# Kernel optimization log

Measured on AMD Instinct MI355X. Metric: run time of the kernel, lower is better.

The kernel has to match this reference:

```python
import jax, jax.numpy as jnp
import numpy as np

N = 2_000_000   # points
C = 65_536      # cluster centers
F = 8           # point feature dim
D = 3           # coord dim


def _dense_params(key, din, dout):
    kw, kb = jax.random.split(key)
    scale = jnp.sqrt(2.0 / din).astype(jnp.float32)
    return (jax.random.normal(kw, (din, dout), jnp.float32) * scale,
            jnp.zeros((dout,), jnp.float32))


def setup_inputs() -> dict:
    key = jax.random.key(0)
    ks = jax.random.split(key, 16)
    inp = {
        "point_features": jax.random.normal(ks[0], (N, F), jnp.float32),
        "labels": jax.random.randint(ks[1], (N,), 0, C, jnp.int32),
        "cluster_centers": jax.random.normal(ks[2], (C, D), jnp.float32),
        "points": jax.random.normal(ks[3], (N, D), jnp.float32),
    }
    # edge MLP: (F+D)->8->16->32->64
    dims = [F + D, 8, 16, 32, 64]
    for i in range(4):
        w, b = _dense_params(ks[4 + i], dims[i], dims[i + 1])
        inp[f"we{i}"] = w
        inp[f"be{i}"] = b
    # attention MLP: (F+D)->64->1
    inp["wa0"], inp["ba0"] = _dense_params(ks[8], F + D, 64)
    inp["wa1"], inp["ba1"] = _dense_params(ks[9], 64, 1)
    # output MLP: 64->128->256
    inp["wo0"], inp["bo0"] = _dense_params(ks[10], 64, 128)
    inp["wo1"], inp["bo1"] = _dense_params(ks[11], 128, 256)
    return inp


def reference(point_features, labels, cluster_centers, points,
              we0, be0, we1, be1, we2, be2, we3, be3,
              wa0, ba0, wa1, ba1, wo0, bo0, wo1, bo1):
    relu = jax.nn.relu
    # gather center coords for each point, build edge input [N, F+D]
    center_coords = cluster_centers[labels]
    x = jnp.concatenate([point_features, center_coords - points], axis=-1)
    # edge MLP 8->16->32->64 (all relu)
    h = relu(x @ we0 + be0)
    h = relu(h @ we1 + be1)
    h = relu(h @ we2 + be2)
    h = relu(h @ we3 + be3)            # [N, 64]
    # attention MLP 64->1 sigmoid
    a = relu(x @ wa0 + ba0)
    a = jax.nn.sigmoid(a @ wa1 + ba1)  # [N, 1]
    t = h * a
    # scatter-sum into clusters
    agg = jax.ops.segment_sum(t, labels, num_segments=C)  # [C, 64]
    # output MLP 128->256 (relu, relu)
    o = relu(agg @ wo0 + bo0)
    o = relu(o @ wo1 + bo1)            # [C, 256]
    return o
```

## Files before the change

### kernel.cpp

```cpp
#include <hip/hip_runtime.h>
#include <hip/hip_bf16.h>
#include <math.h>
#include <stdint.h>

#define TPB 256
#define NCB 32
#define SAGG_LD 68
#define SMID_LD 132

typedef float f32x4 __attribute__((ext_vector_type(4)));
typedef short bf16x8 __attribute__((ext_vector_type(8)));

__device__ inline unsigned int bf16bits(float f)
{
    __hip_bfloat16 b = __float2bfloat16(f);
    return (unsigned int)(*(unsigned short*)&b);
}

__global__ __launch_bounds__(TPB) void hist_kernel(
    const int* __restrict__ labels, int* __restrict__ counts, int n)
{
    int i = blockIdx.x * TPB + threadIdx.x;
    if (i < n) atomicAdd(&counts[labels[i]], 1);
}

__global__ __launch_bounds__(256) void scan_local(
    const int* __restrict__ counts, int* __restrict__ off,
    int* __restrict__ bsum, int C)
{
    __shared__ int sh[256];
    int t = threadIdx.x;
    int i = blockIdx.x * 256 + t;
    int v = (i < C) ? counts[i] : 0;
    sh[t] = v;
    __syncthreads();
    for (int d = 1; d < 256; d <<= 1) {
        int u = (t >= d) ? sh[t - d] : 0;
        __syncthreads();
        sh[t] += u;
        __syncthreads();
    }
    if (i < C) off[i] = sh[t] - v;
    if (t == 255) bsum[blockIdx.x] = sh[255];
}

__global__ __launch_bounds__(256) void scan_base(
    int* __restrict__ bsum, int* __restrict__ off, int nb, int C)
{
    __shared__ int sh[256];
    int t = threadIdx.x;
    int v = (t < nb) ? bsum[t] : 0;
    sh[t] = v;
    __syncthreads();
    for (int d = 1; d < 256; d <<= 1) {
        int u = (t >= d) ? sh[t - d] : 0;
        __syncthreads();
        sh[t] += u;
        __syncthreads();
    }
    if (t < nb) bsum[t] = sh[t] - v;
    if (t == 255) off[C] = sh[255];
}

__global__ __launch_bounds__(256) void scan_apply(
    int* __restrict__ off, int* __restrict__ cursor,
    const int* __restrict__ bsum, int C)
{
    int i = blockIdx.x * 256 + threadIdx.x;
    if (i < C) {
        int v = off[i] + bsum[blockIdx.x];
        off[i] = v;
        cursor[i] = v;
    }
}

__global__ __launch_bounds__(TPB, 4) void point_mlp_kernel(
    const float* __restrict__ pf, const int* __restrict__ labels,
    const float* __restrict__ centers, const float* __restrict__ points,
    const float* __restrict__ we0, const float* __restrict__ be0,
    const float* __restrict__ we1, const float* __restrict__ be1,
    const float* __restrict__ we2, const float* __restrict__ be2,
    const float* __restrict__ we3, const float* __restrict__ be3,
    const float* __restrict__ wa0, const float* __restrict__ ba0,
    const float* __restrict__ wa1, const float* __restrict__ ba1,
    int* __restrict__ cursor, unsigned short* __restrict__ tsort, int n)
{
    __shared__ unsigned int s_h3[4][16][64];

    int i0 = blockIdx.x * TPB + threadIdx.x;
    int i  = (i0 < n) ? i0 : (n - 1);

    float x[11];
    const float4* pf4 = (const float4*)pf;
    float4 p0 = pf4[(size_t)i * 2 + 0];
    float4 p1 = pf4[(size_t)i * 2 + 1];
    x[0] = p0.x; x[1] = p0.y; x[2] = p0.z; x[3] = p0.w;
    x[4] = p1.x; x[5] = p1.y; x[6] = p1.z; x[7] = p1.w;

    int lbl = labels[i];
    x[8]  = centers[lbl * 3 + 0] - points[(size_t)i * 3 + 0];
    x[9]  = centers[lbl * 3 + 1] - points[(size_t)i * 3 + 1];
    x[10] = centers[lbl * 3 + 2] - points[(size_t)i * 3 + 2];

    int pos = 0;
    if (i0 < n) pos = atomicAdd(&cursor[lbl], 1);

    float s = ba1[0];
#pragma unroll
    for (int j = 0; j < 64; j++) {
        float aj = ba0[j];
#pragma unroll
        for (int k = 0; k < 11; k++) aj = fmaf(x[k], wa0[k * 64 + j], aj);
        aj = fmaxf(aj, 0.f);
        s = fmaf(aj, wa1[j], s);
    }
    float gate = 1.f / (1.f + __expf(-s));

    float h1[8];
#pragma unroll
    for (int j = 0; j < 8; j++) {
        float v = be0[j];
#pragma unroll
        for (int k = 0; k < 11; k++) v = fmaf(x[k], we0[k * 8 + j], v);
        h1[j] = fmaxf(v, 0.f);
    }
    float h2[16];
#pragma unroll
    for (int j = 0; j < 16; j++) {
        float v = be1[j];
#pragma unroll
        for (int k = 0; k < 8; k++) v = fmaf(h1[k], we1[k * 16 + j], v);
        h2[j] = fmaxf(v, 0.f);
    }
    float h3[32];
#pragma unroll
    for (int j = 0; j < 32; j++) {
        float v = be2[j];
#pragma unroll
        for (int k = 0; k < 16; k++) v = fmaf(h2[k], we2[k * 32 + j], v);
        h3[j] = fmaxf(v, 0.f);
    }

    int lane = threadIdx.x & 63;
    int w    = threadIdx.x >> 6;
    int lg   = lane >> 4;
    int lm   = lane & 15;
    int pbase = blockIdx.x * TPB + w * 64;

#pragma unroll
    for (int kk = 0; kk < 16; kk++) {
        s_h3[w][kk][lane] = bf16bits(h3[2 * kk]) | (bf16bits(h3[2 * kk + 1]) << 16);
    }

    bf16x8 afrag[4];
#pragma unroll
    for (int mt = 0; mt < 4; mt++) {
        union { unsigned int u[4]; bf16x8 v; } au;
#pragma unroll
        for (int ii = 0; ii < 4; ii++) {
            float w0 = we3[(lg * 8 + 2 * ii + 0) * 64 + mt * 16 + lm];
            float w1 = we3[(lg * 8 + 2 * ii + 1) * 64 + mt * 16 + lm];
            au.u[ii] = bf16bits(w0) | (bf16bits(w1) << 16);
        }
        afrag[mt] = au.v;
    }

#pragma unroll
    for (int nt = 0; nt < 4; nt++) {
        int   spt  = nt * 16 + lm;
        float g    = __shfl(gate, spt, 64);
        int   ppos = __shfl(pos,  spt, 64);
        bool  valid = (pbase + spt) < n;

        union { unsigned int u[4]; bf16x8 v; } bu;
#pragma unroll
        for (int ii = 0; ii < 4; ii++) bu.u[ii] = s_h3[w][lg * 4 + ii][spt];

#pragma unroll
        for (int mt = 0; mt < 4; mt++) {
            f32x4 acc = {0.f, 0.f, 0.f, 0.f};
            acc = __builtin_amdgcn_mfma_f32_16x16x32_bf16(afrag[mt], bu.v, acc, 0, 0, 0);
            int jb = mt * 16 + lg * 4;
            const float4 bias = *(const float4*)&be3[jb];
            float v0 = fmaxf(acc[0] + bias.x, 0.f) * g;
            float v1 = fmaxf(acc[1] + bias.y, 0.f) * g;
            float v2 = fmaxf(acc[2] + bias.z, 0.f) * g;
            float v3 = fmaxf(acc[3] + bias.w, 0.f) * g;
            if (valid) {
                unsigned int d0 = bf16bits(v0) | (bf16bits(v1) << 16);
                unsigned int d1 = bf16bits(v2) | (bf16bits(v3) << 16);
                *(uint2*)((unsigned int*)tsort + (size_t)ppos * 32 + (jb >> 1)) =
                    make_uint2(d0, d1);
            }
        }
    }
}

__global__ __launch_bounds__(TPB) void agg_outmlp_kernel(
    const unsigned short* __restrict__ tsort,
    const int* __restrict__ off,
    const float* __restrict__ wo0, const float* __restrict__ bo0,
    const float* __restrict__ wo1, const float* __restrict__ bo1,
    float* __restrict__ out)
{
    __shared__ float s_agg[NCB * SAGG_LD];
    __shared__ float s_mid[NCB * SMID_LD];
    int tid = threadIdx.x;
    int c0 = blockIdx.x * NCB;

    {
        int lane  = tid & 63;
        int w     = tid >> 6;
        int rlane = lane >> 3;
        int word  = lane & 7;
        const uint4* t128 = (const uint4*)tsort;
#define BF_LO(u) (__uint_as_float((u) << 16))
#define BF_HI(u) (__uint_as_float((u) & 0xffff0000u))
        for (int lc = w * 8; lc < w * 8 + 8; lc++) {
            int rb = off[c0 + lc];
            int re = off[c0 + lc + 1];
            float a[8];
#pragma unroll
            for (int q = 0; q < 8; q++) a[q] = 0.f;
            for (int r = rb; r < re; r += 16) {
                int r0 = r + rlane;
                int r1 = r + 8 + rlane;
                uint4 v0 = make_uint4(0u, 0u, 0u, 0u);
                uint4 v1 = make_uint4(0u, 0u, 0u, 0u);
                if (r0 < re) v0 = t128[(size_t)r0 * 8 + word];
                if (r1 < re) v1 = t128[(size_t)r1 * 8 + word];
                a[0] += BF_LO(v0.x) + BF_LO(v1.x);
                a[1] += BF_HI(v0.x) + BF_HI(v1.x);
                a[2] += BF_LO(v0.y) + BF_LO(v1.y);
                a[3] += BF_HI(v0.y) + BF_HI(v1.y);
                a[4] += BF_LO(v0.z) + BF_LO(v1.z);
                a[5] += BF_HI(v0.z) + BF_HI(v1.z);
                a[6] += BF_LO(v0.w) + BF_LO(v1.w);
                a[7] += BF_HI(v0.w) + BF_HI(v1.w);
            }
#pragma unroll
            for (int m = 8; m < 64; m <<= 1) {
#pragma unroll
                for (int q = 0; q < 8; q++) a[q] += __shfl_xor(a[q], m, 64);
            }
            if (rlane == 0) {
                *(float4*)&s_agg[lc * SAGG_LD + word * 8 + 0] =
                    make_float4(a[0], a[1], a[2], a[3]);
                *(float4*)&s_agg[lc * SAGG_LD + word * 8 + 4] =
                    make_float4(a[4], a[5], a[6], a[7]);
            }
        }
#undef BF_LO
#undef BF_HI
    }
    __syncthreads();

    {
        int mg = tid & 15;
        int cg = tid >> 4;
        int m0 = mg * 8;
        float acc[2][8];
#pragma unroll
        for (int mi = 0; mi < 8; mi++) {
            float b = bo0[m0 + mi];
            acc[0][mi] = b;
            acc[1][mi] = b;
        }
        for (int k = 0; k < 64; k += 4) {
            float4 a0 = *(const float4*)&s_agg[(cg * 2 + 0) * SAGG_LD + k];
            float4 a1 = *(const float4*)&s_agg[(cg * 2 + 1) * SAGG_LD + k];
            float av0[4] = {a0.x, a0.y, a0.z, a0.w};
            float av1[4] = {a1.x, a1.y, a1.z, a1.w};
#pragma unroll
            for (int q = 0; q < 4; q++) {
                float4 wlo = *(const float4*)&wo0[(k + q) * 128 + m0];
                float4 whi = *(const float4*)&wo0[(k + q) * 128 + m0 + 4];
                float wv[8] = {wlo.x, wlo.y, wlo.z, wlo.w,
                               whi.x, whi.y, whi.z, whi.w};
#pragma unroll
                for (int mi = 0; mi < 8; mi++) {
                    acc[0][mi] = fmaf(av0[q], wv[mi], acc[0][mi]);
                    acc[1][mi] = fmaf(av1[q], wv[mi], acc[1][mi]);
                }
            }
        }
#pragma unroll
        for (int c = 0; c < 2; c++) {
            float4 lo = make_float4(fmaxf(acc[c][0], 0.f), fmaxf(acc[c][1], 0.f),
                                    fmaxf(acc[c][2], 0.f), fmaxf(acc[c][3], 0.f));
            float4 hi = make_float4(fmaxf(acc[c][4], 0.f), fmaxf(acc[c][5], 0.f),
                                    fmaxf(acc[c][6], 0.f), fmaxf(acc[c][7], 0.f));
            *(float4*)&s_mid[(cg * 2 + c) * SMID_LD + m0 + 0] = lo;
            *(float4*)&s_mid[(cg * 2 + c) * SMID_LD + m0 + 4] = hi;
        }
    }
    __syncthreads();

    {
        int mg = tid & 31;
        int cg = tid >> 5;
        int m0 = mg * 8;
        float acc[4][8];
#pragma unroll
        for (int mi = 0; mi < 8; mi++) {
            float b = bo1[m0 + mi];
            acc[0][mi] = b;
            acc[1][mi] = b;
            acc[2][mi] = b;
            acc[3][mi] = b;
        }
        for (int j = 0; j < 128; j += 4) {
            float4 a0 = *(const float4*)&s_mid[(cg * 4 + 0) * SMID_LD + j];
            float4 a1 = *(const float4*)&s_mid[(cg * 4 + 1) * SMID_LD + j];
            float4 a2 = *(const float4*)&s_mid[(cg * 4 + 2) * SMID_LD + j];
            float4 a3 = *(const float4*)&s_mid[(cg * 4 + 3) * SMID_LD + j];
            float av0[4] = {a0.x, a0.y, a0.z, a0.w};
            float av1[4] = {a1.x, a1.y, a1.z, a1.w};
            float av2[4] = {a2.x, a2.y, a2.z, a2.w};
            float av3[4] = {a3.x, a3.y, a3.z, a3.w};
#pragma unroll
            for (int q = 0; q < 4; q++) {
                float4 wlo = *(const float4*)&wo1[(j + q) * 256 + m0];
                float4 whi = *(const float4*)&wo1[(j + q) * 256 + m0 + 4];
                float wv[8] = {wlo.x, wlo.y, wlo.z, wlo.w,
                               whi.x, whi.y, whi.z, whi.w};
#pragma unroll
                for (int mi = 0; mi < 8; mi++) {
                    acc[0][mi] = fmaf(av0[q], wv[mi], acc[0][mi]);
                    acc[1][mi] = fmaf(av1[q], wv[mi], acc[1][mi]);
                    acc[2][mi] = fmaf(av2[q], wv[mi], acc[2][mi]);
                    acc[3][mi] = fmaf(av3[q], wv[mi], acc[3][mi]);
                }
            }
        }
#pragma unroll
        for (int c = 0; c < 4; c++) {
            float4 lo = make_float4(fmaxf(acc[c][0], 0.f), fmaxf(acc[c][1], 0.f),
                                    fmaxf(acc[c][2], 0.f), fmaxf(acc[c][3], 0.f));
            float4 hi = make_float4(fmaxf(acc[c][4], 0.f), fmaxf(acc[c][5], 0.f),
                                    fmaxf(acc[c][6], 0.f), fmaxf(acc[c][7], 0.f));
            size_t row = (size_t)(c0 + cg * 4 + c) * 256 + m0;
            *(float4*)&out[row + 0] = lo;
            *(float4*)&out[row + 4] = hi;
        }
    }
}

extern "C" void kernel_launch(void* const* d_in, const int* in_sizes, int n_in,
                              void* d_out, int out_size, void* d_ws, size_t ws_size,
                              hipStream_t stream)
{
    const float* pf      = (const float*)d_in[0];
    const int*   labels  = (const int*)d_in[1];
    const float* centers = (const float*)d_in[2];
    const float* points  = (const float*)d_in[3];
    const float* we0 = (const float*)d_in[4];
    const float* be0 = (const float*)d_in[5];
    const float* we1 = (const float*)d_in[6];
    const float* be1 = (const float*)d_in[7];
    const float* we2 = (const float*)d_in[8];
    const float* be2 = (const float*)d_in[9];
    const float* we3 = (const float*)d_in[10];
    const float* be3 = (const float*)d_in[11];
    const float* wa0 = (const float*)d_in[12];
    const float* ba0 = (const float*)d_in[13];
    const float* wa1 = (const float*)d_in[14];
    const float* ba1 = (const float*)d_in[15];
    const float* wo0 = (const float*)d_in[16];
    const float* bo0 = (const float*)d_in[17];
    const float* wo1 = (const float*)d_in[18];
    const float* bo1 = (const float*)d_in[19];
    float* out = (float*)d_out;

    int n = in_sizes[0] / 8;
    int C = in_sizes[2] / 3;

    int* counts = (int*)d_ws;
    int* cursor = counts + C;
    int* off    = cursor + C;
    int* bsum   = off + C + 1;
    uintptr_t tb = ((uintptr_t)(bsum + 256) + 255) & ~(uintptr_t)255;
    unsigned short* tsort = (unsigned short*)tb;

    hipMemsetAsync(counts, 0, (size_t)C * sizeof(int), stream);

    int pblocks = (n + TPB - 1) / TPB;
    int nb = (C + 255) / 256;
    hist_kernel<<<pblocks, TPB, 0, stream>>>(labels, counts, n);
    scan_local<<<nb, 256, 0, stream>>>(counts, off, bsum, C);
    scan_base<<<1, 256, 0, stream>>>(bsum, off, nb, C);
    scan_apply<<<nb, 256, 0, stream>>>(off, cursor, bsum, C);

    point_mlp_kernel<<<pblocks, TPB, 0, stream>>>(
        pf, labels, centers, points,
        we0, be0, we1, be1, we2, be2, we3, be3,
        wa0, ba0, wa1, ba1, cursor, tsort, n);

    agg_outmlp_kernel<<<C / NCB, TPB, 0, stream>>>(
        tsort, off, wo0, bo0, wo1, bo1, out);
}
```

Measured before the change: 557.5 us.

## Move attention MLP and edge layer 2 onto bf16 MFMA via LDS staging

The per-thread scalar FP32 attention MLP (11->64->1) and the 16->32 edge layer are replaced with 16x16x32 bf16 MFMA tiles. Inputs are staged in LDS as packed bf16 per wave. The gate is reduced across lanes with xor shuffles and kept per output tile. This removes most of the per-point VALU FMA work, which likely dominated the point kernel, but lowers precision of the attention input and layer 2 to bf16. It also adds extra LDS traffic and doubles the shared buffer.

```diff
diff --git a/kernel.cpp b/kernel.cpp
--- a/kernel.cpp
+++ b/kernel.cpp
@@ -15,6 +15,11 @@
 {
     __hip_bfloat16 b = __float2bfloat16(f);
     return (unsigned int)(*(unsigned short*)&b);
+}
+
+__device__ inline unsigned int bfpack(float lo, float hi)
+{
+    return bf16bits(lo) | (bf16bits(hi) << 16);
 }
 
 __global__ __launch_bounds__(TPB) void hist_kernel(
@@ -85,9 +90,16 @@
     const float* __restrict__ wa1, const float* __restrict__ ba1,
     int* __restrict__ cursor, unsigned short* __restrict__ tsort, int n)
 {
-    __shared__ unsigned int s_h3[4][16][64];
-
-    int i0 = blockIdx.x * TPB + threadIdx.x;
+    __shared__ unsigned int s_stage[4][32][64];
+
+    int tid  = threadIdx.x;
+    int lane = tid & 63;
+    int w    = tid >> 6;
+    int lg   = lane >> 4;
+    int lm   = lane & 15;
+    int pbase = blockIdx.x * TPB + w * 64;
+
+    int i0 = blockIdx.x * TPB + tid;
     int i  = (i0 < n) ? i0 : (n - 1);
 
     float x[11];
@@ -105,16 +117,13 @@
     int pos = 0;
     if (i0 < n) pos = atomicAdd(&cursor[lbl], 1);
 
-    float s = ba1[0];
-#pragma unroll
-    for (int j = 0; j < 64; j++) {
-        float aj = ba0[j];
-#pragma unroll
-        for (int k = 0; k < 11; k++) aj = fmaf(x[k], wa0[k * 64 + j], aj);
-        aj = fmaxf(aj, 0.f);
-        s = fmaf(aj, wa1[j], s);
-    }
-    float gate = 1.f / (1.f + __expf(-s));
+#pragma unroll
+    for (int r = 0; r < 16; r++) {
+        unsigned int v = 0;
+        if (2 * r < 11)     v  = bf16bits(x[2 * r]);
+        if (2 * r + 1 < 11) v |= bf16bits(x[2 * r + 1]) << 16;
+        s_stage[w][r][lane] = v;
+    }
 
     float h1[8];
 #pragma unroll
@@ -132,54 +141,119 @@
         for (int k = 0; k < 8; k++) v = fmaf(h1[k], we1[k * 16 + j], v);
         h2[j] = fmaxf(v, 0.f);
     }
-    float h3[32];
-#pragma unroll
-    for (int j = 0; j < 32; j++) {
-        float v = be2[j];
-#pragma unroll
-        for (int k = 0; k < 16; k++) v = fmaf(h2[k], we2[k * 32 + j], v);
-        h3[j] = fmaxf(v, 0.f);
-    }
-
-    int lane = threadIdx.x & 63;
-    int w    = threadIdx.x >> 6;
-    int lg   = lane >> 4;
-    int lm   = lane & 15;
-    int pbase = blockIdx.x * TPB + w * 64;
-
-#pragma unroll
-    for (int kk = 0; kk < 16; kk++) {
-        s_h3[w][kk][lane] = bf16bits(h3[2 * kk]) | (bf16bits(h3[2 * kk + 1]) << 16);
-    }
-
-    bf16x8 afrag[4];
+
+    bf16x8 a_at[4];
 #pragma unroll
     for (int mt = 0; mt < 4; mt++) {
         union { unsigned int u[4]; bf16x8 v; } au;
 #pragma unroll
         for (int ii = 0; ii < 4; ii++) {
-            float w0 = we3[(lg * 8 + 2 * ii + 0) * 64 + mt * 16 + lm];
-            float w1 = we3[(lg * 8 + 2 * ii + 1) * 64 + mt * 16 + lm];
-            au.u[ii] = bf16bits(w0) | (bf16bits(w1) << 16);
-        }
-        afrag[mt] = au.v;
-    }
-
+            int k0 = lg * 8 + 2 * ii;
+            int j  = mt * 16 + lm;
+            unsigned int u = 0;
+            if (k0 < 11)     u  = bf16bits(wa0[k0 * 64 + j]);
+            if (k0 + 1 < 11) u |= bf16bits(wa0[(k0 + 1) * 64 + j]) << 16;
+            au.u[ii] = u;
+        }
+        a_at[mt] = au.v;
+    }
+
+    float gate_arr[4];
 #pragma unroll
     for (int nt = 0; nt < 4; nt++) {
-        int   spt  = nt * 16 + lm;
-        float g    = __shfl(gate, spt, 64);
-        int   ppos = __shfl(pos,  spt, 64);
-        bool  valid = (pbase + spt) < n;
-
+        int spt = nt * 16 + lm;
         union { unsigned int u[4]; bf16x8 v; } bu;
 #pragma unroll
-        for (int ii = 0; ii < 4; ii++) bu.u[ii] = s_h3[w][lg * 4 + ii][spt];
-
+        for (int ii = 0; ii < 4; ii++) bu.u[ii] = s_stage[w][lg * 4 + ii][spt];
+
+        float part = 0.f;
 #pragma unroll
         for (int mt = 0; mt < 4; mt++) {
             f32x4 acc = {0.f, 0.f, 0.f, 0.f};
-            acc = __builtin_amdgcn_mfma_f32_16x16x32_bf16(afrag[mt], bu.v, acc, 0, 0, 0);
+            acc = __builtin_amdgcn_mfma_f32_16x16x32_bf16(a_at[mt], bu.v, acc, 0, 0, 0);
+            int jb = mt * 16 + lg * 4;
+            const float4 b0 = *(const float4*)&ba0[jb];
+            const float4 w1 = *(const float4*)&wa1[jb];
+            part = fmaf(fmaxf(acc[0] + b0.x, 0.f), w1.x, part);
+            part = fmaf(fmaxf(acc[1] + b0.y, 0.f), w1.y, part);
+            part = fmaf(fmaxf(acc[2] + b0.z, 0.f), w1.z, part);
+            part = fmaf(fmaxf(acc[3] + b0.w, 0.f), w1.w, part);
+        }
+        part += __shfl_xor(part, 16, 64);
+        part += __shfl_xor(part, 32, 64);
+        float s = ba1[0] + part;
+        gate_arr[nt] = 1.f / (1.f + __expf(-s));
+    }
+
+#pragma unroll
+    for (int r = 0; r < 8; r++)
+        s_stage[w][r][lane] = bfpack(h2[2 * r], h2[2 * r + 1]);
+
+    bf16x8 a_l2[2];
+#pragma unroll
+    for (int mt = 0; mt < 2; mt++) {
+        union { unsigned int u[4]; bf16x8 v; } au;
+#pragma unroll
+        for (int ii = 0; ii < 4; ii++) {
+            int k0 = lg * 8 + 2 * ii;
+            int j  = mt * 16 + lm;
+            unsigned int u = 0;
+            if (k0 < 16)     u  = bf16bits(we2[k0 * 32 + j]);
+            if (k0 + 1 < 16) u |= bf16bits(we2[(k0 + 1) * 32 + j]) << 16;
+            au.u[ii] = u;
+        }
+        a_l2[mt] = au.v;
+    }
+
+#pragma unroll
+    for (int nt = 0; nt < 4; nt++) {
+        int spt = nt * 16 + lm;
+        union { unsigned int u[4]; bf16x8 v; } bu;
+#pragma unroll
+        for (int ii = 0; ii < 4; ii++) bu.u[ii] = s_stage[w][lg * 4 + ii][spt];
+
+#pragma unroll
+        for (int mt = 0; mt < 2; mt++) {
+            f32x4 acc = {0.f, 0.f, 0.f, 0.f};
+            acc = __builtin_amdgcn_mfma_f32_16x16x32_bf16(a_l2[mt], bu.v, acc, 0, 0, 0);
+            const float4 b2 = *(const float4*)&be2[mt * 16 + lg * 4];
+            float d0 = fmaxf(acc[0] + b2.x, 0.f);
+            float d1 = fmaxf(acc[1] + b2.y, 0.f);
+            float d2 = fmaxf(acc[2] + b2.z, 0.f);
+            float d3 = fmaxf(acc[3] + b2.w, 0.f);
+            s_stage[w][16 + mt * 8 + lg * 2 + 0][spt] = bfpack(d0, d1);
+            s_stage[w][16 + mt * 8 + lg * 2 + 1][spt] = bfpack(d2, d3);
+        }
+    }
+
+    bf16x8 a_l3[4];
+#pragma unroll
+    for (int mt = 0; mt < 4; mt++) {
+        union { unsigned int u[4]; bf16x8 v; } au;
+#pragma unroll
+        for (int ii = 0; ii < 4; ii++) {
+            int k0 = lg * 8 + 2 * ii;
+            int j  = mt * 16 + lm;
+            au.u[ii] = bfpack(we3[k0 * 64 + j], we3[(k0 + 1) * 64 + j]);
+        }
+        a_l3[mt] = au.v;
+    }
+
+#pragma unroll
+    for (int nt = 0; nt < 4; nt++) {
+        int   spt   = nt * 16 + lm;
+        float g     = gate_arr[nt];
+        int   ppos  = __shfl(pos, spt, 64);
+        bool  valid = (pbase + spt) < n;
+
+        union { unsigned int u[4]; bf16x8 v; } bu;
+#pragma unroll
+        for (int ii = 0; ii < 4; ii++) bu.u[ii] = s_stage[w][16 + lg * 4 + ii][spt];
+
+#pragma unroll
+        for (int mt = 0; mt < 4; mt++) {
+            f32x4 acc = {0.f, 0.f, 0.f, 0.f};
+            acc = __builtin_amdgcn_mfma_f32_16x16x32_bf16(a_l3[mt], bu.v, acc, 0, 0, 0);
             int jb = mt * 16 + lg * 4;
             const float4 bias = *(const float4*)&be3[jb];
             float v0 = fmaxf(acc[0] + bias.x, 0.f) * g;
@@ -187,8 +261,8 @@
             float v2 = fmaxf(acc[2] + bias.z, 0.f) * g;
             float v3 = fmaxf(acc[3] + bias.w, 0.f) * g;
             if (valid) {
-                unsigned int d0 = bf16bits(v0) | (bf16bits(v1) << 16);
-                unsigned int d1 = bf16bits(v2) | (bf16bits(v3) << 16);
+                unsigned int d0 = bfpack(v0, v1);
+                unsigned int d1 = bfpack(v2, v3);
                 *(uint2*)((unsigned int*)tsort + (size_t)ppos * 32 + (jb >> 1)) =
                     make_uint2(d0, d1);
             }
```

After: 595.7 us. +6.8%, slower.
